# Optimization experiments

Measured on AMD Instinct MI355X. Metric: run time of the kernel, lower is better.

## Reference

```python
import jax, jax.numpy as jnp
import numpy as np

D_MODEL, D_K, D_V = 512, 64, 64


def setup_inputs() -> dict:
    key = jax.random.key(0)
    ks = jax.random.split(key, 9)
    b, n = 8, 4096
    scale = 1.0 / np.sqrt(D_MODEL)
    return {
        "q": jax.random.normal(ks[0], (b, n, D_MODEL), jnp.float32),
        "k": jax.random.normal(ks[1], (b, n, D_MODEL), jnp.float32),
        "v": jax.random.normal(ks[2], (b, n, D_MODEL), jnp.float32),
        "Wq": jax.random.normal(ks[3], (D_MODEL, D_K), jnp.float32) * scale,
        "bq": jnp.zeros((D_K,), jnp.float32),
        "Wk": jax.random.normal(ks[4], (D_MODEL, D_K), jnp.float32) * scale,
        "bk": jnp.zeros((D_K,), jnp.float32),
        "Wv": jax.random.normal(ks[5], (D_MODEL, D_V), jnp.float32) * scale,
        "bv": jnp.zeros((D_V,), jnp.float32),
        "mask": 0,
    }


def reference(q, k, v, Wq, bq, Wk, bk, Wv, bv, mask):
    # linear projections (torch Linear: x @ W^T + b; here W stored as [in,out])
    qp = jnp.einsum("bnd,de->bne", q, Wq) + bq  # (b,n,d_k)
    kp = jnp.einsum("bnd,de->bne", k, Wk) + bk  # (b,n,d_k)
    vp = jnp.einsum("bnd,de->bne", v, Wv) + bv  # (b,n,d_v)
    temper = D_K ** 0.5
    attn = jnp.einsum("bqe,bke->bqk", qp, kp) / temper  # (b,n,n)
    # original: attn[attn == mask] = -inf (equality mask on scores)
    attn = jnp.where(attn == jnp.float32(mask), -jnp.inf, attn)
    # NOTE: original's `attn.masked_fill(look_ahead_mask==0, -inf)` is NOT
    # in-place and its result is discarded, so look_ahead_mask has no effect.
    attn = jax.nn.softmax(attn, axis=-1)
    return jnp.einsum("bqk,bkv->bqv", attn, vp)  # (b,n,d_v)
```

## Files before the change

kernel.cpp:

```cpp
#include <hip/hip_runtime.h>

typedef _Float16 f16;
typedef _Float16 f16x2 __attribute__((ext_vector_type(2)));
typedef _Float16 f16x4 __attribute__((ext_vector_type(4)));
typedef _Float16 f16x8 __attribute__((ext_vector_type(8)));
typedef __fp16   h16x2 __attribute__((ext_vector_type(2)));
typedef float    f32x4 __attribute__((ext_vector_type(4)));
typedef float    f32x16 __attribute__((ext_vector_type(16)));

static constexpr float L2E = 1.44269504088896340736f;
static constexpr float QSC = 0.18033688011112042f;

static __device__ __forceinline__ f32x4 mfma16(f16x8 a, f16x8 b, f32x4 c) {
    return __builtin_amdgcn_mfma_f32_16x16x32_f16(a, b, c, 0, 0, 0);
}
static __device__ __forceinline__ f32x16 mfma32(f16x8 a, f16x8 b, f32x16 c) {
    return __builtin_amdgcn_mfma_f32_32x32x16_f16(a, b, c, 0, 0, 0);
}
static __device__ __forceinline__ f16x2 cvt_pk(float a, float b) {
    h16x2 t = __builtin_amdgcn_cvt_pkrtz(a, b);
    return __builtin_bit_cast(f16x2, t);
}
static __device__ __forceinline__ void gload16(const void* g, void* l) {
    __builtin_amdgcn_global_load_lds(
        (const __attribute__((address_space(1))) unsigned int*)g,
        (__attribute__((address_space(3))) unsigned int*)l, 16, 0, 0);
}

__global__ void ah_wt_prep(const float* __restrict__ Wq,
                           const float* __restrict__ Wk,
                           const float* __restrict__ Wv,
                           f16* __restrict__ WT) {
    const float* W = (blockIdx.x == 0) ? Wq : (blockIdx.x == 1) ? Wk : Wv;
    f16* o = WT + (size_t)blockIdx.x * (64 * 512);
    for (int i = threadIdx.x; i < 64 * 512; i += blockDim.x) {
        int col = i >> 9, e = i & 511;
        o[i] = (f16)W[e * 64 + col];
    }
}

__global__ __launch_bounds__(256, 3) void ah_proj(
    const float* __restrict__ Xq, const float* __restrict__ Xk, const float* __restrict__ Xv,
    const float* __restrict__ bq, const float* __restrict__ bk, const float* __restrict__ bv,
    const f16* __restrict__ WT,
    f16* __restrict__ qp, f16* __restrict__ kp, f16* __restrict__ vpT) {

    const int tens = blockIdx.y;
    const float* X    = (tens == 0) ? Xq : (tens == 1) ? Xk : Xv;
    const float* bias = (tens == 0) ? bq : (tens == 1) ? bk : bv;
    const f16* wt = WT + (size_t)tens * (64 * 512);
    const float osc = (tens == 0) ? QSC : 1.0f;

    const int lane = threadIdx.x & 63;
    const int wave = threadIdx.x >> 6;
    const int l15 = lane & 15, g = lane >> 4;
    const int row0 = blockIdx.x * 64;
    const int wrow = wave * 16;

    __shared__ __align__(16) char smem[49152];

    const int xr8 = lane >> 3;
    const int xsu = (lane & 7) ^ xr8;

#define PSTAGE(KC) do {                                                              \
    char* _xb = smem + ((KC) & 3) * 12288;                                           \
    char* _wb = _xb + 8192;                                                          \
    gload16(X + (size_t)(row0 + wrow + xr8) * 512 + (KC) * 32 + xsu * 4,             \
            _xb + wave * 2048);                                                      \
    gload16(X + (size_t)(row0 + wrow + 8 + xr8) * 512 + (KC) * 32 + xsu * 4,         \
            _xb + wave * 2048 + 1024);                                               \
    gload16(wt + (size_t)(wrow + (lane >> 2)) * 512 + (KC) * 32 + (lane & 3) * 8,    \
            _wb + wave * 1024);                                                      \
} while (0)

    f32x4 acc[4];
#pragma unroll
    for (int b = 0; b < 4; ++b) acc[b] = (f32x4){0.f, 0.f, 0.f, 0.f};

#define PCOMP(KC) do {                                                               \
    const char* _xb = smem + ((KC) & 3) * 12288;                                     \
    const char* _wb = _xb + 8192;                                                    \
    const char* _cb = _xb + (wrow + l15) * 128;                                      \
    float4 v0 = *(const float4*)(_cb + (((2 * g + 0) ^ (l15 & 7)) << 4));            \
    float4 v1 = *(const float4*)(_cb + (((2 * g + 1) ^ (l15 & 7)) << 4));            \
    f16x2 p0 = cvt_pk(v0.x, v0.y), p1 = cvt_pk(v0.z, v0.w);                          \
    f16x2 p2 = cvt_pk(v1.x, v1.y), p3 = cvt_pk(v1.z, v1.w);                          \
    f16x8 a;                                                                         \
    a[0] = p0[0]; a[1] = p0[1]; a[2] = p1[0]; a[3] = p1[1];                          \
    a[4] = p2[0]; a[5] = p2[1]; a[6] = p3[0]; a[7] = p3[1];                          \
    _Pragma("unroll")                                                                \
    for (int cf = 0; cf < 4; ++cf) {                                                 \
        f16x8 bfr = *(const f16x8*)(_wb + (cf * 16 + l15) * 64 + g * 16);            \
        acc[cf] = mfma16(a, bfr, acc[cf]);                                           \
    }                                                                                \
} while (0)

    PSTAGE(0); PSTAGE(1); PSTAGE(2);
    for (int kc = 0; kc < 13; ++kc) {
        PSTAGE(kc + 3);
        asm volatile("s_waitcnt vmcnt(9)" ::: "memory");
        __builtin_amdgcn_sched_barrier(0);
        __builtin_amdgcn_s_barrier();
        __builtin_amdgcn_sched_barrier(0);
        PCOMP(kc);
        __builtin_amdgcn_sched_barrier(0);
        __builtin_amdgcn_s_barrier();
    }
    asm volatile("s_waitcnt vmcnt(6)" ::: "memory");
    __builtin_amdgcn_sched_barrier(0);
    __builtin_amdgcn_s_barrier();
    PCOMP(13);
    __builtin_amdgcn_s_barrier();
    asm volatile("s_waitcnt vmcnt(3)" ::: "memory");
    __builtin_amdgcn_sched_barrier(0);
    __builtin_amdgcn_s_barrier();
    PCOMP(14);
    __builtin_amdgcn_s_barrier();
    asm volatile("s_waitcnt vmcnt(0)" ::: "memory");
    __builtin_amdgcn_sched_barrier(0);
    __builtin_amdgcn_s_barrier();
    PCOMP(15);
    __syncthreads();
#undef PSTAGE
#undef PCOMP

    f16* lds = (f16*)smem;
#pragma unroll
    for (int cf = 0; cf < 4; ++cf) {
        float b = bias[cf * 16 + l15];
#pragma unroll
        for (int r = 0; r < 4; ++r) {
            int rr = wrow + g * 4 + r;
            lds[rr * 68 + cf * 16 + l15] = (f16)((acc[cf][r] + b) * osc);
        }
    }
    __syncthreads();

    if (tens < 2) {
        f16* o = ((tens == 0) ? qp : kp) + (size_t)row0 * 64;
        for (int c = threadIdx.x; c < 64 * 16; c += 256) {
            int r = c >> 4, ch = c & 15;
            *(f16x4*)(o + r * 64 + ch * 4) = *(const f16x4*)(&lds[r * 68 + ch * 4]);
        }
    } else {
        int b = row0 >> 12, n0 = row0 & 4095;
        f16* o = vpT + (size_t)b * 64 * 4096 + n0;
        for (int c = threadIdx.x; c < 64 * 16; c += 256) {
            int d = c >> 4, nch = c & 15;
            f16x4 v;
#pragma unroll
            for (int j = 0; j < 4; ++j) v[j] = lds[(nch * 4 + j) * 68 + d];
            *(f16x4*)(o + (size_t)d * 4096 + nch * 4) = v;
        }
    }
}

__global__ __launch_bounds__(512, 2) void ah_attn(
    const f16* __restrict__ qp, const f16* __restrict__ kp, const f16* __restrict__ vpT,
    const int* __restrict__ maskp, float* __restrict__ out) {

    const int id = blockIdx.x;
    const int batch = id & 7, qtile = id >> 3;
    const int lane = threadIdx.x & 63, wave = threadIdx.x >> 6;
    const int l31 = lane & 31, hi2 = lane >> 5;
    const int s = wave & 3, qg = wave >> 2;
    const int q0 = qtile * 128 + qg * 64;
    const float mthr = L2E * (float)maskp[0];

    const f16* qpb = qp + (size_t)batch * 4096 * 64;
    const f16* kpb = kp + (size_t)batch * 4096 * 64;
    const f16* vpb = vpT + (size_t)batch * 64 * 4096;

    __shared__ __align__(16) char smem[65536];
    __shared__ float mlx[2][4][2][32];

    const int krow = lane >> 3;
    const int vrow = lane >> 2;
    const int eswzK = (lane & 7) ^ krow;
    const int eswzV = (lane & 3) ^ (vrow & 3);
    const int swzK = l31 & 7, swzV = l31 & 3;

#define STAGE(DB, IT) do {                                                          \
    const int _k0 = (((IT) * 4 + s) << 5);                                          \
    char* _b = smem + ((s * 2 + (DB)) * 8192) + (qg ? 4096 : 0);                    \
    if (qg == 0) {                                                                  \
        _Pragma("unroll")                                                           \
        for (int _j = 0; _j < 4; ++_j)                                              \
            gload16(kpb + (size_t)(_k0 + _j * 8 + krow) * 64 + eswzK * 8,           \
                    _b + _j * 1024);                                                \
    } else {                                                                        \
        _Pragma("unroll")                                                           \
        for (int _j = 0; _j < 4; ++_j)                                              \
            gload16(vpb + (size_t)(_j * 16 + vrow) * 4096 + _k0 + eswzV * 8,        \
                    _b + _j * 1024);                                                \
    }                                                                               \
} while (0)

    f16x8 qf_[2][4];
#pragma unroll
    for (int qt = 0; qt < 2; ++qt)
#pragma unroll
        for (int st = 0; st < 4; ++st)
            qf_[qt][st] = *(const f16x8*)(qpb + (size_t)(q0 + qt * 32 + l31) * 64 + st * 16 + hi2 * 8);

    f32x16 oacc[2][2];
#pragma unroll
    for (int dt = 0; dt < 2; ++dt)
#pragma unroll
        for (int qt = 0; qt < 2; ++qt)
#pragma unroll
            for (int r = 0; r < 16; ++r) oacc[dt][qt][r] = 0.f;
    float ps[2] = {0.f, 0.f};

    STAGE(0, 0);
    int db = 0;
    for (int it = 0; it < 32; ++it) {
        if (it < 31) {
            STAGE(db ^ 1, it + 1);
            asm volatile("s_waitcnt vmcnt(4)" ::: "memory");
        } else {
            asm volatile("s_waitcnt vmcnt(0)" ::: "memory");
        }
        __builtin_amdgcn_s_barrier();
        __builtin_amdgcn_sched_barrier(0);

        const char* kb = smem + (s * 2 + db) * 8192;
        const char* vb = kb + 4096;

        f16x8 ka[4];
#pragma unroll
        for (int st = 0; st < 4; ++st)
            ka[st] = *(const f16x8*)(kb + l31 * 128 + (((st * 2 + hi2) ^ swzK) << 4));
        f32x16 sacc[2];
#pragma unroll
        for (int qt = 0; qt < 2; ++qt)
#pragma unroll
            for (int r = 0; r < 16; ++r) sacc[qt][r] = 0.f;
#pragma unroll
        for (int st = 0; st < 4; ++st)
#pragma unroll
            for (int qt = 0; qt < 2; ++qt)
                sacc[qt] = mfma32(ka[st], qf_[qt][st], sacc[qt]);

        f16x8 av[2][2];
#pragma unroll
        for (int dt = 0; dt < 2; ++dt)
#pragma unroll
            for (int t = 0; t < 2; ++t) {
                const char* p = vb + (dt * 32 + l31) * 64 + hi2 * 8;
                *(f16x4*)(&av[dt][t])       = *(const f16x4*)(p + (((t * 2 + 0) ^ swzV) << 4));
                *((f16x4*)(&av[dt][t]) + 1) = *(const f16x4*)(p + (((t * 2 + 1) ^ swzV) << 4));
            }

        f16x8 pb_[2][2];
#pragma unroll
        for (int qt = 0; qt < 2; ++qt)
#pragma unroll
            for (int t = 0; t < 2; ++t)
#pragma unroll
                for (int w = 0; w < 4; ++w) {
                    float s0 = sacc[qt][t * 8 + 2 * w];
                    float s1 = sacc[qt][t * 8 + 2 * w + 1];
                    float e0 = __builtin_amdgcn_exp2f(s0);
                    float e1 = __builtin_amdgcn_exp2f(s1);
                    float p0 = (s0 == mthr) ? 0.f : e0;
                    float p1 = (s1 == mthr) ? 0.f : e1;
                    ps[qt] += p0 + p1;
                    ((f16x2*)(&pb_[qt][t]))[w] = cvt_pk(p0, p1);
                }

#pragma unroll
        for (int dt = 0; dt < 2; ++dt)
#pragma unroll
            for (int qt = 0; qt < 2; ++qt)
#pragma unroll
                for (int t = 0; t < 2; ++t)
                    oacc[dt][qt] = mfma32(av[dt][t], pb_[qt][t], oacc[dt][qt]);

        __builtin_amdgcn_sched_barrier(0);
        __builtin_amdgcn_s_barrier();
        __builtin_amdgcn_sched_barrier(0);
        db ^= 1;
    }
#undef STAGE

    ps[0] += __shfl_xor(ps[0], 32);
    ps[1] += __shfl_xor(ps[1], 32);
    if (lane < 32) { mlx[qg][s][0][lane] = ps[0]; mlx[qg][s][1][lane] = ps[1]; }
    __syncthreads();

    float* SC = (float*)smem;
#define SCI(B, DT, QT, R) ((((qg * 2 + (B)) * 64) + ((DT) * 2 + (QT)) * 16 + (R)) * 64 + lane)
    if (s >= 2) {
#pragma unroll
        for (int dt = 0; dt < 2; ++dt)
#pragma unroll
            for (int qt = 0; qt < 2; ++qt)
#pragma unroll
                for (int r = 0; r < 16; ++r)
                    SC[SCI(s - 2, dt, qt, r)] = oacc[dt][qt][r];
    }
    __syncthreads();
    if (s < 2) {
#pragma unroll
        for (int dt = 0; dt < 2; ++dt)
#pragma unroll
            for (int qt = 0; qt < 2; ++qt)
#pragma unroll
                for (int r = 0; r < 16; ++r)
                    oacc[dt][qt][r] += SC[SCI(s, dt, qt, r)];
        if (s == 1) {
#pragma unroll
            for (int dt = 0; dt < 2; ++dt)
#pragma unroll
                for (int qt = 0; qt < 2; ++qt)
#pragma unroll
                    for (int r = 0; r < 16; ++r)
                        SC[SCI(1, dt, qt, r)] = oacc[dt][qt][r];
        }
    }
    __syncthreads();
    if (s == 0) {
        float inv[2];
#pragma unroll
        for (int qt = 0; qt < 2; ++qt)
            inv[qt] = 1.0f / (mlx[qg][0][qt][l31] + mlx[qg][1][qt][l31] +
                              mlx[qg][2][qt][l31] + mlx[qg][3][qt][l31]);
#pragma unroll
        for (int qt = 0; qt < 2; ++qt) {
            float* o0 = out + ((size_t)batch * 4096 + q0 + qt * 32 + l31) * 64;
#pragma unroll
            for (int dt = 0; dt < 2; ++dt)
#pragma unroll
                for (int rg = 0; rg < 4; ++rg) {
                    float4 v;
                    v.x = (oacc[dt][qt][rg * 4 + 0] + SC[SCI(1, dt, qt, rg * 4 + 0)]) * inv[qt];
                    v.y = (oacc[dt][qt][rg * 4 + 1] + SC[SCI(1, dt, qt, rg * 4 + 1)]) * inv[qt];
                    v.z = (oacc[dt][qt][rg * 4 + 2] + SC[SCI(1, dt, qt, rg * 4 + 2)]) * inv[qt];
                    v.w = (oacc[dt][qt][rg * 4 + 3] + SC[SCI(1, dt, qt, rg * 4 + 3)]) * inv[qt];
                    *(float4*)(o0 + dt * 32 + rg * 8 + hi2 * 4) = v;
                }
        }
    }
#undef SCI
}

extern "C" void kernel_launch(void* const* d_in, const int* in_sizes, int n_in,
                              void* d_out, int out_size, void* d_ws, size_t ws_size,
                              hipStream_t stream) {
    const float* q  = (const float*)d_in[0];
    const float* k  = (const float*)d_in[1];
    const float* v  = (const float*)d_in[2];
    const float* Wq = (const float*)d_in[3];
    const float* bq = (const float*)d_in[4];
    const float* Wk = (const float*)d_in[5];
    const float* bk = (const float*)d_in[6];
    const float* Wv = (const float*)d_in[7];
    const float* bv = (const float*)d_in[8];
    const int* mask = (const int*)d_in[9];
    float* out = (float*)d_out;

    const size_t NTOK = (size_t)8 * 4096;
    f16* qp  = (f16*)d_ws;
    f16* kp  = qp + NTOK * 64;
    f16* vpT = kp + NTOK * 64;
    f16* WT  = vpT + NTOK * 64;

    ah_wt_prep<<<dim3(3), 256, 0, stream>>>(Wq, Wk, Wv, WT);
    ah_proj<<<dim3(512, 3), 256, 0, stream>>>(q, k, v, bq, bk, bv, WT, qp, kp, vpT);
    ah_attn<<<dim3(256), 512, 0, stream>>>(qp, kp, vpT, mask, out);
}
```

Before: 115.8 us.

## Use double-buffered 64-wide K chunks in projection kernel instead of 4-stage 32-wide

The projection GEMM now stages 64 columns of K per step in two LDS buffers, replacing 32-column steps in a four-deep ring. This halves the number of loop iterations and barrier pairs, and each step issues more MFMAs per synchronization. The swizzle patterns for the X and W tiles are changed to match the wider rows. The trade-off is less prefetch depth (one stage ahead instead of three), which may expose more global-load latency.

```diff
diff --git a/kernel.cpp b/kernel.cpp
--- a/kernel.cpp
+++ b/kernel.cpp
@@ -59,70 +59,76 @@
 
     __shared__ __align__(16) char smem[49152];
 
-    const int xr8 = lane >> 3;
-    const int xsu = (lane & 7) ^ xr8;
+    const int xrow4 = lane >> 4;
+    const int xr7   = xrow4 & 7;
+    const int wrow8 = lane >> 3;
 
 #define PSTAGE(KC) do {                                                              \
-    char* _xb = smem + ((KC) & 3) * 12288;                                           \
-    char* _wb = _xb + 8192;                                                          \
-    gload16(X + (size_t)(row0 + wrow + xr8) * 512 + (KC) * 32 + xsu * 4,             \
-            _xb + wave * 2048);                                                      \
-    gload16(X + (size_t)(row0 + wrow + 8 + xr8) * 512 + (KC) * 32 + xsu * 4,         \
-            _xb + wave * 2048 + 1024);                                               \
-    gload16(wt + (size_t)(wrow + (lane >> 2)) * 512 + (KC) * 32 + (lane & 3) * 8,    \
-            _wb + wave * 1024);                                                      \
-} while (0)
-
-    f32x4 acc[4];
-#pragma unroll
-    for (int b = 0; b < 4; ++b) acc[b] = (f32x4){0.f, 0.f, 0.f, 0.f};
-
-#define PCOMP(KC) do {                                                               \
-    const char* _xb = smem + ((KC) & 3) * 12288;                                     \
-    const char* _wb = _xb + 8192;                                                    \
-    const char* _cb = _xb + (wrow + l15) * 128;                                      \
-    float4 v0 = *(const float4*)(_cb + (((2 * g + 0) ^ (l15 & 7)) << 4));            \
-    float4 v1 = *(const float4*)(_cb + (((2 * g + 1) ^ (l15 & 7)) << 4));            \
-    f16x2 p0 = cvt_pk(v0.x, v0.y), p1 = cvt_pk(v0.z, v0.w);                          \
-    f16x2 p2 = cvt_pk(v1.x, v1.y), p3 = cvt_pk(v1.z, v1.w);                          \
-    f16x8 a;                                                                         \
-    a[0] = p0[0]; a[1] = p0[1]; a[2] = p1[0]; a[3] = p1[1];                          \
-    a[4] = p2[0]; a[5] = p2[1]; a[6] = p3[0]; a[7] = p3[1];                          \
+    char* _xb = smem + ((KC) & 1) * 24576;                                           \
+    char* _wb = _xb + 16384;                                                         \
     _Pragma("unroll")                                                                \
-    for (int cf = 0; cf < 4; ++cf) {                                                 \
-        f16x8 bfr = *(const f16x8*)(_wb + (cf * 16 + l15) * 64 + g * 16);            \
-        acc[cf] = mfma16(a, bfr, acc[cf]);                                           \
+    for (int _j = 0; _j < 4; ++_j) {                                                 \
+        int _r7 = (_j * 4 + xrow4) & 7;                                              \
+        gload16(X + (size_t)(row0 + wrow + _j * 4 + xrow4) * 512 + (KC) * 64 +       \
+                    (((lane & 15) ^ _r7) << 2),                                      \
+                _xb + (wrow + _j * 4) * 256);                                        \
+    }                                                                                \
+    _Pragma("unroll")                                                                \
+    for (int _m = 0; _m < 2; ++_m) {                                                 \
+        int _r7 = (_m * 8 + wrow8) & 7;                                              \
+        gload16(wt + (size_t)(wave * 16 + _m * 8 + wrow8) * 512 + (KC) * 64 +        \
+                    (((lane & 7) ^ _r7) << 3),                                       \
+                _wb + (wave * 16 + _m * 8) * 128);                                   \
     }                                                                                \
 } while (0)
 
-    PSTAGE(0); PSTAGE(1); PSTAGE(2);
-    for (int kc = 0; kc < 13; ++kc) {
-        PSTAGE(kc + 3);
-        asm volatile("s_waitcnt vmcnt(9)" ::: "memory");
+    f32x4 acc[4];
+#pragma unroll
+    for (int b = 0; b < 4; ++b) acc[b] = (f32x4){0.f, 0.f, 0.f, 0.f};
+
+#define PCOMP(KC) do {                                                               \
+    const char* _xb = smem + ((KC) & 1) * 24576;                                     \
+    const char* _wb = _xb + 16384;                                                   \
+    const char* _xr = _xb + (wrow + l15) * 256;                                      \
+    const int _s7 = l15 & 7;                                                         \
+    _Pragma("unroll")                                                                \
+    for (int ec = 0; ec < 2; ++ec) {                                                 \
+        int u0 = ec * 8 + g * 2;                                                     \
+        float4 v0 = *(const float4*)(_xr + (((u0 + 0) ^ _s7) << 4));                 \
+        float4 v1 = *(const float4*)(_xr + (((u0 + 1) ^ _s7) << 4));                 \
+        f16x2 p0 = cvt_pk(v0.x, v0.y), p1 = cvt_pk(v0.z, v0.w);                      \
+        f16x2 p2 = cvt_pk(v1.x, v1.y), p3 = cvt_pk(v1.z, v1.w);                      \
+        f16x8 a;                                                                     \
+        a[0] = p0[0]; a[1] = p0[1]; a[2] = p1[0]; a[3] = p1[1];                      \
+        a[4] = p2[0]; a[5] = p2[1]; a[6] = p3[0]; a[7] = p3[1];                      \
+        _Pragma("unroll")                                                            \
+        for (int cf = 0; cf < 4; ++cf) {                                             \
+            f16x8 bfr = *(const f16x8*)(_wb + (cf * 16 + l15) * 128 +                \
+                                        (((ec * 4 + g) ^ _s7) << 4));                \
+            acc[cf] = mfma16(a, bfr, acc[cf]);                                       \
+        }                                                                            \
+    }                                                                                \
+} while (0)
+
+    PSTAGE(0);
+    for (int kc = 0; kc < 8; ++kc) {
+        if (kc < 7) {
+            PSTAGE(kc + 1);
+            asm volatile("s_waitcnt vmcnt(6)" ::: "memory");
+        } else {
+            asm volatile("s_waitcnt vmcnt(0)" ::: "memory");
+        }
         __builtin_amdgcn_sched_barrier(0);
         __builtin_amdgcn_s_barrier();
         __builtin_amdgcn_sched_barrier(0);
         PCOMP(kc);
         __builtin_amdgcn_sched_barrier(0);
         __builtin_amdgcn_s_barrier();
-    }
-    asm volatile("s_waitcnt vmcnt(6)" ::: "memory");
-    __builtin_amdgcn_sched_barrier(0);
-    __builtin_amdgcn_s_barrier();
-    PCOMP(13);
-    __builtin_amdgcn_s_barrier();
-    asm volatile("s_waitcnt vmcnt(3)" ::: "memory");
-    __builtin_amdgcn_sched_barrier(0);
-    __builtin_amdgcn_s_barrier();
-    PCOMP(14);
-    __builtin_amdgcn_s_barrier();
-    asm volatile("s_waitcnt vmcnt(0)" ::: "memory");
-    __builtin_amdgcn_sched_barrier(0);
-    __builtin_amdgcn_s_barrier();
-    PCOMP(15);
-    __syncthreads();
+        __builtin_amdgcn_sched_barrier(0);
+    }
 #undef PSTAGE
 #undef PCOMP
+    __syncthreads();
 
     f16* lds = (f16*)smem;
 #pragma unroll
```

Result: no change. 118.1 us (+2.0%).
